# Performance work log

Measured on AMD Instinct MI355X. Metric: run time of the kernel, lower is better.

Reference implementation:

```python
import math
import jax, jax.numpy as jnp
import numpy as np

H, N2, B, L = 1024, 32, 8, 4096  # d_model, d_state//2, batch, seq len


def setup_inputs() -> dict:
    key = jax.random.key(0)
    ks = jax.random.split(key, 6)
    log_dt = jax.random.uniform(ks[0], (H,)) * (math.log(0.1) - math.log(0.001)) + math.log(0.001)
    C_real = jax.random.normal(ks[1], (H, N2, 2))  # view_as_real of complex C
    log_A_real = jnp.log(0.5 * jnp.ones((H, N2)))  # 'exp' parameterization
    A_imag = math.pi * jnp.tile(jnp.arange(N2, dtype=jnp.float32), (H, 1))
    D = jax.random.normal(ks[2], (H,))
    W_out = jax.random.normal(ks[3], (2 * H, H)) * 0.02  # Conv1d(h, 2h, 1) weight
    b_out = jnp.zeros((2 * H,))
    u = jax.random.normal(ks[4], (B, H, L))
    return {"u": u, "log_dt": log_dt, "C_real": C_real, "log_A_real": log_A_real,
            "A_imag": A_imag, "D": D, "W_out": W_out, "b_out": b_out}


def reference(u, log_dt, C_real, log_A_real, A_imag, D, W_out, b_out):
    Lx = u.shape[-1]
    # --- kernel generation (S4D 'exp' parameterization) ---
    dt = jnp.exp(log_dt)                                   # (H,)
    C = C_real[..., 0] + 1j * C_real[..., 1]               # (H, N2) complex
    A = -jnp.exp(log_A_real) + 1j * A_imag                 # (H, N2) complex
    dtA = A * dt[:, None]                                  # (H, N2)
    K = dtA[:, :, None] * jnp.arange(Lx)                   # (H, N2, L)
    Cmod = C * (jnp.exp(dtA) - 1.0) / A
    k = 2.0 * jnp.einsum('hn,hnl->hl', Cmod, jnp.exp(K)).real  # (H, L)
    # --- FFT long convolution ---
    k_f = jnp.fft.rfft(k, n=2 * Lx)                        # (H, L+1)
    u_f = jnp.fft.rfft(u, n=2 * Lx)                        # (B, H, L+1)
    y = jnp.fft.irfft(u_f * k_f, n=2 * Lx)[..., :Lx]       # (B, H, L)
    # --- skip, activation, GLU output projection (Conv1d k=1 == matmul) ---
    y = y + u * D[:, None]
    y = jax.nn.gelu(y, approximate=False)  # torch nn.GELU default is exact erf
    z = jnp.einsum('oh,bhl->bol', W_out, y) + b_out[:, None]  # (B, 2H, L)
    a, g = jnp.split(z, 2, axis=-2)  # GLU along channel dim (-2)
    return a * jax.nn.sigmoid(g)
```

## Files before the change

kernel.cpp:

```cpp
#include <hip/hip_runtime.h>
#include <hip/hip_bf16.h>
#include <math.h>


#define H_DIM 1024
#define N2_DIM 32
#define B_DIM 8
#define L_DIM 4096

typedef __attribute__((ext_vector_type(8))) short short8v;
typedef __attribute__((ext_vector_type(4))) float f32x4;

#define GLOAD16(g, l) __builtin_amdgcn_global_load_lds( \
    (const __attribute__((address_space(1))) unsigned int*)(g), \
    (__attribute__((address_space(3))) unsigned int*)(l), 16, 0, 0)

__device__ __forceinline__ unsigned short f2bf(float x) {
  unsigned int v = __float_as_uint(x);
  unsigned int r = (v + 0x7fff + ((v >> 16) & 1)) >> 16;
  return (unsigned short)r;
}

__global__ __launch_bounds__(256) void prep_tables(
    const float* __restrict__ log_dt, const float* __restrict__ C_real,
    const float* __restrict__ log_A_real, const float* __restrict__ A_imag,
    float2* __restrict__ wtab, float2* __restrict__ ctab, float2* __restrict__ mtab) {
  int idx = blockIdx.x * 256 + threadIdx.x;
  int h = idx >> 5;
  double dt = exp((double)log_dt[h]);
  double Ar = -exp((double)log_A_real[idx]);
  double Ai = (double)A_imag[idx];
  double xr = dt * Ar, xi = dt * Ai;
  double er = exp(xr);
  double wr = er * cos(xi), wi = er * sin(xi);
  wtab[idx] = make_float2((float)wr, (float)wi);
  double crr = (double)C_real[2 * idx], cii = (double)C_real[2 * idx + 1];
  double nr = wr - 1.0, ni = wi;
  double den = Ar * Ar + Ai * Ai;
  double qr = (nr * Ar + ni * Ai) / den, qi = (ni * Ar - nr * Ai) / den;
  ctab[idx] = make_float2((float)(2.0 * (crr * qr - cii * qi)),
                          (float)(2.0 * (crr * qi + cii * qr)));
#pragma unroll
  for (int s = 0; s < 6; s++) {
    double p = (double)(64 << s);
    double pr = exp(p * xr);
    mtab[idx * 6 + s] = make_float2((float)(pr * cos(p * xi)), (float)(pr * sin(p * xi)));
  }
}

__global__ __launch_bounds__(256) void prep_w(const float* __restrict__ W,
                                              unsigned short* __restrict__ Wbf) {
  int i = blockIdx.x * 256 + threadIdx.x;
  float4 v = ((const float4*)W)[i];
  ushort4 o;
  o.x = f2bf(v.x); o.y = f2bf(v.y); o.z = f2bf(v.z); o.w = f2bf(v.w);
  ((ushort4*)Wbf)[i] = o;
}

__global__ __launch_bounds__(128) void scan_kernel(
    const float* __restrict__ u, const float2* __restrict__ wtab,
    const float2* __restrict__ ctab, const float2* __restrict__ mtab,
    const float* __restrict__ D, unsigned short* __restrict__ yws) {
  __shared__ float ubuf[64][68];
  __shared__ float ybuf[2][64][68];
  int bh = blockIdx.x;
  int h = bh & (H_DIM - 1);
  int tid = threadIdx.x, lane = tid & 63, wv = tid >> 6;

  const float4* urow = (const float4*)(u + (size_t)bh * L_DIM);
#pragma unroll
  for (int it = 0; it < 8; it++) {
    int i4 = it * 128 + tid;
    float4 v = urow[i4];
    *(float4*)&ubuf[i4 >> 4][(i4 & 15) * 4] = v;
  }

  float wr[16], wi[16], cr[16], ci[16];
  int nbase = h * N2_DIM + wv * 16;
#pragma unroll
  for (int nn = 0; nn < 16; nn++) {
    float2 a = wtab[nbase + nn]; wr[nn] = a.x; wi[nn] = a.y;
    float2 c = ctab[nbase + nn]; cr[nn] = c.x; ci[nn] = c.y;
  }
  __syncthreads();

  float Sr[16], Si[16];
#pragma unroll
  for (int nn = 0; nn < 16; nn++) { Sr[nn] = 0.f; Si[nn] = 0.f; }
  for (int i4 = 0; i4 < 16; i4++) {
    float4 uv = *(float4*)&ubuf[lane][i4 * 4];
#pragma unroll
    for (int e = 0; e < 4; e++) {
      float u_ = (e == 0) ? uv.x : (e == 1) ? uv.y : (e == 2) ? uv.z : uv.w;
#pragma unroll
      for (int nn = 0; nn < 16; nn++) {
        float t = fmaf(-wi[nn], Si[nn], u_);
        float sr = fmaf(wr[nn], Sr[nn], t);
        float si = fmaf(wi[nn], Sr[nn], wr[nn] * Si[nn]);
        Sr[nn] = sr; Si[nn] = si;
      }
    }
  }

#pragma unroll
  for (int s = 0; s < 6; s++) {
    int d = 1 << s;
#pragma unroll
    for (int nn = 0; nn < 16; nn++) {
      float2 m = mtab[(nbase + nn) * 6 + s];
      float rr = __shfl_up(Sr[nn], d, 64);
      float ri = __shfl_up(Si[nn], d, 64);
      rr = (lane >= d) ? rr : 0.f;
      ri = (lane >= d) ? ri : 0.f;
      Sr[nn] = fmaf(m.x, rr, fmaf(-m.y, ri, Sr[nn]));
      Si[nn] = fmaf(m.x, ri, fmaf(m.y, rr, Si[nn]));
    }
  }
#pragma unroll
  for (int nn = 0; nn < 16; nn++) {
    float er = __shfl_up(Sr[nn], 1, 64);
    float ei = __shfl_up(Si[nn], 1, 64);
    Sr[nn] = lane ? er : 0.f;
    Si[nn] = lane ? ei : 0.f;
  }

  for (int i4 = 0; i4 < 16; i4++) {
    float4 uv = *(float4*)&ubuf[lane][i4 * 4];
    float yv[4];
#pragma unroll
    for (int e = 0; e < 4; e++) {
      float u_ = (e == 0) ? uv.x : (e == 1) ? uv.y : (e == 2) ? uv.z : uv.w;
      float yacc = 0.f;
#pragma unroll
      for (int nn = 0; nn < 16; nn++) {
        float t = fmaf(-wi[nn], Si[nn], u_);
        float sr = fmaf(wr[nn], Sr[nn], t);
        float si = fmaf(wi[nn], Sr[nn], wr[nn] * Si[nn]);
        Sr[nn] = sr; Si[nn] = si;
        yacc = fmaf(cr[nn], sr, fmaf(-ci[nn], si, yacc));
      }
      yv[e] = yacc;
    }
    float4 st; st.x = yv[0]; st.y = yv[1]; st.z = yv[2]; st.w = yv[3];
    *(float4*)&ybuf[wv][lane][i4 * 4] = st;
  }
  __syncthreads();

  float Dh = D[h];
#pragma unroll
  for (int it = 0; it < 8; it++) {
    int i4 = it * 128 + tid;
    int row = i4 >> 4, c4 = (i4 & 15) * 4;
    float4 p0 = *(float4*)&ybuf[0][row][c4];
    float4 p1 = *(float4*)&ybuf[1][row][c4];
    float4 uu = *(float4*)&ubuf[row][c4];
    ushort4 st;
    {
      float y = p0.x + p1.x + Dh * uu.x;
      st.x = f2bf(0.5f * y * (1.f + erff(y * 0.70710678118654752f)));
      y = p0.y + p1.y + Dh * uu.y;
      st.y = f2bf(0.5f * y * (1.f + erff(y * 0.70710678118654752f)));
      y = p0.z + p1.z + Dh * uu.z;
      st.z = f2bf(0.5f * y * (1.f + erff(y * 0.70710678118654752f)));
      y = p0.w + p1.w + Dh * uu.w;
      st.w = f2bf(0.5f * y * (1.f + erff(y * 0.70710678118654752f)));
    }
    *(ushort4*)(yws + (size_t)bh * L_DIM + i4 * 4) = st;
  }
}

__global__ __launch_bounds__(256) void transpose_kernel(
    const unsigned short* __restrict__ yws, unsigned short* __restrict__ yT) {
  __shared__ unsigned short tile[64][68];
  int bid = blockIdx.x;
  int lb = bid & 63, hb = (bid >> 6) & 15, b = bid >> 10;
  int h0 = hb * 64, l0 = lb * 64, tid = threadIdx.x;
#pragma unroll
  for (int it = 0; it < 4; it++) {
    int i4 = it * 256 + tid;
    int hr = i4 >> 4, c4 = (i4 & 15) * 4;
    ushort4 v = *(const ushort4*)(yws + ((size_t)(b * H_DIM + h0 + hr)) * L_DIM + l0 + c4);
    *(ushort4*)&tile[hr][c4] = v;
  }
  __syncthreads();
#pragma unroll
  for (int it = 0; it < 4; it++) {
    int i4 = it * 256 + tid;
    int lr = i4 >> 4, hc = (i4 & 15) * 4;
    ushort4 o;
    o.x = tile[hc + 0][lr]; o.y = tile[hc + 1][lr];
    o.z = tile[hc + 2][lr]; o.w = tile[hc + 3][lr];
    *(ushort4*)(yT + ((size_t)(b * L_DIM + l0 + lr)) * H_DIM + h0 + hc) = o;
  }
}

__global__ __launch_bounds__(256) void gemm_kernel(
    const unsigned short* __restrict__ Wbf, const unsigned short* __restrict__ yT,
    const float* __restrict__ b_out, float* __restrict__ out) {
  __shared__ char smem[2][2][16384] __attribute__((aligned(16)));
  int bid = blockIdx.x;
  int swz = (bid & 7) * 512 + (bid >> 3);
  int mb = swz & 15, nb = swz >> 4;
  int m0 = mb * 64;
  int n0 = nb * 128;
  int b = n0 >> 12, l0 = n0 & (L_DIM - 1);
  int tid = threadIdx.x, lane = tid & 63, wid = tid >> 6;
  int wm = wid >> 1, wn = wid & 1;

  const char* Abase = (const char*)Wbf;
  const char* Bbase = (const char*)yT + ((size_t)b * L_DIM + l0) * 2048;
  int rsub = lane >> 3;
  int csw = ((lane & 7) ^ rsub) * 16;

  f32x4 acc[4][4];
#pragma unroll
  for (int i = 0; i < 4; i++)
#pragma unroll
    for (int j = 0; j < 4; j++) acc[i][j] = (f32x4)0.f;

  int rowA[4], rowB[4];
#pragma unroll
  for (int ar = 0; ar < 4; ar++) {
    int f = 2 * wm + (ar & 1) + (ar >> 1) * 4;
    rowA[ar] = (f * 16 + (lane & 15)) * 128;
  }
#pragma unroll
  for (int bn = 0; bn < 4; bn++) {
    rowB[bn] = ((wn * 4 + bn) * 16 + (lane & 15)) * 128;
  }
  int koff = (lane >> 4) * 16;
  int sw = (lane & 7) << 4;

  const char* gsrc;
  char* ldst;
  if (wid == 0) {
    gsrc = Abase + (size_t)(m0 + rsub) * 2048 + csw;
    ldst = (char*)smem + 0 * 16384 + lane * 16;
  } else if (wid == 1) {
    gsrc = Abase + (size_t)(1024 + m0 + rsub) * 2048 + csw;
    ldst = (char*)smem + 0 * 16384 + 8192 + lane * 16;
  } else if (wid == 2) {
    gsrc = Bbase + (size_t)rsub * 2048 + csw;
    ldst = (char*)smem + 1 * 16384 + lane * 16;
  } else {
    gsrc = Bbase + (size_t)(64 + rsub) * 2048 + csw;
    ldst = (char*)smem + 1 * 16384 + 8192 + lane * 16;
  }

#pragma unroll
  for (int i = 0; i < 8; i++) GLOAD16(gsrc + (size_t)i * 8 * 2048, ldst + i * 1024);

  for (int ks = 0; ks < 16; ks++) {
    __syncthreads();
    int cur = ks & 1;
    if (ks < 15) {
      const char* g = gsrc + (size_t)(ks + 1) * 128;
      char* l = ldst + (cur ^ 1) * 32768;
#pragma unroll
      for (int i = 0; i < 8; i++) GLOAD16(g + (size_t)i * 8 * 2048, l + i * 1024);
    }
    const char* LA = smem[cur][0];
    const char* LB = smem[cur][1];
#pragma unroll
    for (int ksl = 0; ksl < 2; ksl++) {
      int kb = (ksl * 64 + koff) ^ sw;
      short8v av[4], bv[4];
#pragma unroll
      for (int ar = 0; ar < 4; ar++) av[ar] = *(const short8v*)(LA + rowA[ar] + kb);
#pragma unroll
      for (int bn = 0; bn < 4; bn++) bv[bn] = *(const short8v*)(LB + rowB[bn] + kb);
#pragma unroll
      for (int ar = 0; ar < 4; ar++)
#pragma unroll
        for (int bn = 0; bn < 4; bn++)
          acc[ar][bn] = __builtin_amdgcn_mfma_f32_16x16x32_bf16(av[ar], bv[bn], acc[ar][bn], 0, 0, 0);
    }
  }

#pragma unroll
  for (int q = 0; q < 2; q++) {
    int obase = m0 + (2 * wm + q) * 16 + (lane >> 4) * 4;
    float4 ba = *(const float4*)&b_out[obase];
    float4 bg = *(const float4*)&b_out[1024 + obase];
    float bav[4] = {ba.x, ba.y, ba.z, ba.w};
    float bgv[4] = {bg.x, bg.y, bg.z, bg.w};
#pragma unroll
    for (int bn = 0; bn < 4; bn++) {
      int col = l0 + (wn * 4 + bn) * 16 + (lane & 15);
      float* op = out + ((size_t)b * H_DIM + obase) * L_DIM + col;
#pragma unroll
      for (int r = 0; r < 4; r++) {
        float a_ = acc[q][bn][r] + bav[r];
        float g_ = acc[q + 2][bn][r] + bgv[r];
        op[(size_t)r * L_DIM] = a_ * (1.f / (1.f + expf(-g_)));
      }
    }
  }
}

extern "C" void kernel_launch(void* const* d_in, const int* in_sizes, int n_in,
                              void* d_out, int out_size, void* d_ws, size_t ws_size,
                              hipStream_t stream) {
  const float* u          = (const float*)d_in[0];
  const float* log_dt     = (const float*)d_in[1];
  const float* C_real     = (const float*)d_in[2];
  const float* log_A_real = (const float*)d_in[3];
  const float* A_imag     = (const float*)d_in[4];
  const float* D          = (const float*)d_in[5];
  const float* W_out      = (const float*)d_in[6];
  const float* b_out      = (const float*)d_in[7];
  float* out = (float*)d_out;

  char* ws = (char*)d_ws;
  float2* wtab = (float2*)(ws + 0);
  float2* ctab = (float2*)(ws + (1 << 18));
  float2* mtab = (float2*)(ws + (1 << 19));
  unsigned short* Wbf = (unsigned short*)(ws + (2 << 20));
  unsigned short* yws = (unsigned short*)(ws + (8ull << 20));
  unsigned short* yT  = (unsigned short*)(ws + (76ull << 20));

  prep_tables<<<128, 256, 0, stream>>>(log_dt, C_real, log_A_real, A_imag, wtab, ctab, mtab);
  prep_w<<<2048, 256, 0, stream>>>(W_out, Wbf);
  scan_kernel<<<B_DIM * H_DIM, 128, 0, stream>>>(u, wtab, ctab, mtab, D, yws);
  transpose_kernel<<<8192, 256, 0, stream>>>(yws, yT);
  gemm_kernel<<<4096, 256, 0, stream>>>(Wbf, yT, b_out, out);
}
```

Baseline: 748.8 us.

## Fuse scan epilogue into chunked loop, swizzle LDS, shrink ybuf for occupancy

The second scan pass now works in chunks of 8 timesteps. Wave 0 writes its partial outputs to a small double-buffered LDS slot, and wave 1 adds them to its own partials, applies the D skip and GELU, and stores bf16 directly. The large ybuf and the separate epilogue pass go away. The ubuf column index is XOR-swizzled to avoid LDS bank conflicts on the strided row reads, and launch bounds request 3 blocks per CU. The trade-offs are a barrier per chunk, the epilogue serialised onto one wave, and less-coalesced global stores (each lane writes 8 bytes 128 bytes apart).

```diff
diff --git a/kernel.cpp b/kernel.cpp
--- a/kernel.cpp
+++ b/kernel.cpp
@@ -19,6 +19,10 @@
   unsigned int v = __float_as_uint(x);
   unsigned int r = (v + 0x7fff + ((v >> 16) & 1)) >> 16;
   return (unsigned short)r;
+}
+
+__device__ __forceinline__ float gelu_exact(float y) {
+  return 0.5f * y * (1.f + erff(y * 0.70710678118654752f));
 }
 
 __global__ __launch_bounds__(256) void prep_tables(
@@ -57,12 +61,12 @@
   ((ushort4*)Wbf)[i] = o;
 }
 
-__global__ __launch_bounds__(128) void scan_kernel(
+__global__ __launch_bounds__(128, 3) void scan_kernel(
     const float* __restrict__ u, const float2* __restrict__ wtab,
     const float2* __restrict__ ctab, const float2* __restrict__ mtab,
     const float* __restrict__ D, unsigned short* __restrict__ yws) {
   __shared__ float ubuf[64][68];
-  __shared__ float ybuf[2][64][68];
+  __shared__ float ybuf[2][64][12];
   int bh = blockIdx.x;
   int h = bh & (H_DIM - 1);
   int tid = threadIdx.x, lane = tid & 63, wv = tid >> 6;
@@ -72,7 +76,8 @@
   for (int it = 0; it < 8; it++) {
     int i4 = it * 128 + tid;
     float4 v = urow[i4];
-    *(float4*)&ubuf[i4 >> 4][(i4 & 15) * 4] = v;
+    int r = i4 >> 4, c = i4 & 15;
+    *(float4*)&ubuf[r][(c ^ ((r >> 3) & 7)) * 4] = v;
   }
 
   float wr[16], wi[16], cr[16], ci[16];
@@ -84,11 +89,13 @@
   }
   __syncthreads();
 
+  int lsw = (lane >> 3) & 7;
+
   float Sr[16], Si[16];
 #pragma unroll
   for (int nn = 0; nn < 16; nn++) { Sr[nn] = 0.f; Si[nn] = 0.f; }
   for (int i4 = 0; i4 < 16; i4++) {
-    float4 uv = *(float4*)&ubuf[lane][i4 * 4];
+    float4 uv = *(float4*)&ubuf[lane][(i4 ^ lsw) * 4];
 #pragma unroll
     for (int e = 0; e < 4; e++) {
       float u_ = (e == 0) ? uv.x : (e == 1) ? uv.y : (e == 2) ? uv.z : uv.w;
@@ -124,48 +131,51 @@
     Si[nn] = lane ? ei : 0.f;
   }
 
-  for (int i4 = 0; i4 < 16; i4++) {
-    float4 uv = *(float4*)&ubuf[lane][i4 * 4];
-    float yv[4];
-#pragma unroll
-    for (int e = 0; e < 4; e++) {
-      float u_ = (e == 0) ? uv.x : (e == 1) ? uv.y : (e == 2) ? uv.z : uv.w;
-      float yacc = 0.f;
-#pragma unroll
-      for (int nn = 0; nn < 16; nn++) {
-        float t = fmaf(-wi[nn], Si[nn], u_);
-        float sr = fmaf(wr[nn], Sr[nn], t);
-        float si = fmaf(wi[nn], Sr[nn], wr[nn] * Si[nn]);
-        Sr[nn] = sr; Si[nn] = si;
-        yacc = fmaf(cr[nn], sr, fmaf(-ci[nn], si, yacc));
+  float Dh = D[h];
+  for (int p = 0; p < 8; p++) {
+    float yv[2][4];
+    float4 uq[2];
+#pragma unroll
+    for (int q = 0; q < 2; q++) {
+      int i4 = 2 * p + q;
+      float4 uv = *(float4*)&ubuf[lane][(i4 ^ lsw) * 4];
+      uq[q] = uv;
+#pragma unroll
+      for (int e = 0; e < 4; e++) {
+        float u_ = (e == 0) ? uv.x : (e == 1) ? uv.y : (e == 2) ? uv.z : uv.w;
+        float yacc = 0.f;
+#pragma unroll
+        for (int nn = 0; nn < 16; nn++) {
+          float t = fmaf(-wi[nn], Si[nn], u_);
+          float sr = fmaf(wr[nn], Sr[nn], t);
+          float si = fmaf(wi[nn], Sr[nn], wr[nn] * Si[nn]);
+          Sr[nn] = sr; Si[nn] = si;
+          yacc = fmaf(cr[nn], sr, fmaf(-ci[nn], si, yacc));
+        }
+        yv[q][e] = yacc;
       }
-      yv[e] = yacc;
-    }
-    float4 st; st.x = yv[0]; st.y = yv[1]; st.z = yv[2]; st.w = yv[3];
-    *(float4*)&ybuf[wv][lane][i4 * 4] = st;
-  }
-  __syncthreads();
-
-  float Dh = D[h];
-#pragma unroll
-  for (int it = 0; it < 8; it++) {
-    int i4 = it * 128 + tid;
-    int row = i4 >> 4, c4 = (i4 & 15) * 4;
-    float4 p0 = *(float4*)&ybuf[0][row][c4];
-    float4 p1 = *(float4*)&ybuf[1][row][c4];
-    float4 uu = *(float4*)&ubuf[row][c4];
-    ushort4 st;
-    {
-      float y = p0.x + p1.x + Dh * uu.x;
-      st.x = f2bf(0.5f * y * (1.f + erff(y * 0.70710678118654752f)));
-      y = p0.y + p1.y + Dh * uu.y;
-      st.y = f2bf(0.5f * y * (1.f + erff(y * 0.70710678118654752f)));
-      y = p0.z + p1.z + Dh * uu.z;
-      st.z = f2bf(0.5f * y * (1.f + erff(y * 0.70710678118654752f)));
-      y = p0.w + p1.w + Dh * uu.w;
-      st.w = f2bf(0.5f * y * (1.f + erff(y * 0.70710678118654752f)));
-    }
-    *(ushort4*)(yws + (size_t)bh * L_DIM + i4 * 4) = st;
+    }
+    if (wv == 0) {
+      float4 s0; s0.x = yv[0][0]; s0.y = yv[0][1]; s0.z = yv[0][2]; s0.w = yv[0][3];
+      float4 s1; s1.x = yv[1][0]; s1.y = yv[1][1]; s1.z = yv[1][2]; s1.w = yv[1][3];
+      *(float4*)&ybuf[p & 1][lane][0] = s0;
+      *(float4*)&ybuf[p & 1][lane][4] = s1;
+    }
+    __syncthreads();
+    if (wv == 1) {
+#pragma unroll
+      for (int q = 0; q < 2; q++) {
+        float4 p0 = *(float4*)&ybuf[p & 1][lane][q * 4];
+        float4 uu = uq[q];
+        ushort4 st;
+        float y;
+        y = p0.x + yv[q][0] + Dh * uu.x; st.x = f2bf(gelu_exact(y));
+        y = p0.y + yv[q][1] + Dh * uu.y; st.y = f2bf(gelu_exact(y));
+        y = p0.z + yv[q][2] + Dh * uu.z; st.z = f2bf(gelu_exact(y));
+        y = p0.w + yv[q][3] + Dh * uu.w; st.w = f2bf(gelu_exact(y));
+        *(ushort4*)(yws + (size_t)bh * L_DIM + lane * 64 + (2 * p + q) * 4) = st;
+      }
+    }
   }
 }
 
```

Result: faster. 711.2 us (-5.0%).
